# Kernel optimization log

Hardware: AMD Instinct MI355X
Metric: run time of the kernel (lower is better)

## Reference

```python
import math
import jax, jax.numpy as jnp
import numpy as np

B, Q, K, N, F = 4096, 1024, 256, 16384, 512


def setup_inputs() -> dict:
    key = jax.random.key(0)
    ks = jax.random.split(key, 6)
    return {
        "pooled_h": jax.random.normal(ks[0], (B, Q), jnp.float32),
        "snapshot_keys": jax.random.normal(ks[1], (N, K), jnp.float32),
        "snapshot_embs": jax.random.normal(ks[2], (N, F), jnp.float32),
        "Wq": jax.random.normal(ks[3], (Q, K), jnp.float32) / math.sqrt(Q),
        "bq": jnp.zeros((K,), jnp.float32),
        "Wb": jax.random.normal(ks[4], (Q, 1), jnp.float32) / math.sqrt(Q),
        "bb": jnp.zeros((1,), jnp.float32),
        "fallback": jnp.zeros((F,), jnp.float32),
        "topk": 2,
    }


def reference(pooled_h, snapshot_keys, snapshot_embs, Wq, bq, Wb, bb, fallback, topk):
    # q = q_proj(pooled_h)                                  [B, K]
    q = pooled_h @ Wq + bq
    # scores = q @ keys^T / sqrt(key_dim)                   [B, N]
    scores = (q @ snapshot_keys.T) / jnp.sqrt(jnp.asarray(q.shape[-1], q.dtype))
    # top-k values/indices per row, scatter into -inf mask, masked softmax
    vals, idx = jax.lax.top_k(scores, topk)                 # [B, k], [B, k]
    rows = jnp.arange(scores.shape[0])[:, None]             # [B, 1]
    mask = jnp.full_like(scores, -jnp.inf).at[rows, idx].set(vals)
    alpha = jax.nn.softmax(mask, axis=-1)                   # [B, N], k nonzeros/row
    emb_mix = alpha @ snapshot_embs                         # [B, F]
    beta = jax.nn.sigmoid(pooled_h @ Wb + bb)               # [B, 1]
    return emb_mix * beta, alpha
```

## Files before the change

kernel.cpp:

```cpp
#include <hip/hip_runtime.h>
#include <math.h>

#define B_ 4096
#define Q_ 1024
#define KD 256
#define N_ 16384
#define F_ 512

typedef __attribute__((ext_vector_type(8))) short bhalf8;
typedef __attribute__((ext_vector_type(4))) float f32x4;
typedef __attribute__((ext_vector_type(16))) float f32x16;

static __device__ __forceinline__ unsigned short f2bf(float f) {
  unsigned int u = __builtin_bit_cast(unsigned int, f);
  unsigned int r = (u + 0x7fffu + ((u >> 16) & 1u)) >> 16;
  return (unsigned short)r;
}
static __device__ __forceinline__ unsigned umaxu(unsigned a, unsigned b) { return a > b ? a : b; }
static __device__ __forceinline__ unsigned uminu(unsigned a, unsigned b) { return a < b ? a : b; }

__global__ __launch_bounds__(256)
void k_convert_keys(const float* __restrict__ keys, unsigned short* __restrict__ kbf) {
  const size_t base = ((size_t)blockIdx.x * 256 + threadIdx.x) * 8;
  const float4 x = *reinterpret_cast<const float4*>(&keys[base]);
  const float4 y = *reinterpret_cast<const float4*>(&keys[base + 4]);
  bhalf8 o;
  o[0] = (short)f2bf(x.x); o[1] = (short)f2bf(x.y);
  o[2] = (short)f2bf(x.z); o[3] = (short)f2bf(x.w);
  o[4] = (short)f2bf(y.x); o[5] = (short)f2bf(y.y);
  o[6] = (short)f2bf(y.z); o[7] = (short)f2bf(y.w);
  *reinterpret_cast<bhalf8*>(&kbf[base]) = o;
}

__global__ __launch_bounds__(256, 2)
void k_qproj(const float* __restrict__ ph, const float* __restrict__ Wq,
             float* __restrict__ qpart) {
  __shared__ __align__(16) float As[2][64][64];
  __shared__ __align__(16) float Ws[2][64][64];
  const int tid = threadIdx.x;
  const int tx = tid & 15, ty = tid >> 4;
  const int c0 = (blockIdx.x & 3) * 64;
  const int kh = blockIdx.x >> 2;
  const int r0 = blockIdx.y * 64;
  const int kbase = kh * 512;
  const int sr = tid & 63, sk = (tid >> 6) * 16;
  float* qout = qpart + (size_t)kh * B_ * KD;

  float acc[4][4] = {};
  float4 a0, a1, a2, a3;

  auto stageW = [&](int bi, int kc) {
#pragma unroll
    for (int i = 0; i < 4; ++i) {
      const int D = i * 4096 + tid * 16;
      const int kk = D >> 8;
      const int cb = D & 255;
      const float* src = &Wq[(size_t)(kbase + kc * 64 + kk) * KD + c0 + (cb >> 2)];
      __builtin_amdgcn_global_load_lds(
          (const __attribute__((address_space(1))) unsigned int*)src,
          (__attribute__((address_space(3))) unsigned int*)((char*)&Ws[bi][0][0] + D),
          16, 0, 0);
    }
  };

  stageW(0, 0);
  {
    const float* src = &ph[(size_t)(r0 + sr) * Q_ + kbase + sk];
    a0 = *reinterpret_cast<const float4*>(src + 0);
    a1 = *reinterpret_cast<const float4*>(src + 4);
    a2 = *reinterpret_cast<const float4*>(src + 8);
    a3 = *reinterpret_cast<const float4*>(src + 12);
    As[0][sk + 0][sr] = a0.x; As[0][sk + 1][sr] = a0.y;
    As[0][sk + 2][sr] = a0.z; As[0][sk + 3][sr] = a0.w;
    As[0][sk + 4][sr] = a1.x; As[0][sk + 5][sr] = a1.y;
    As[0][sk + 6][sr] = a1.z; As[0][sk + 7][sr] = a1.w;
    As[0][sk + 8][sr] = a2.x; As[0][sk + 9][sr] = a2.y;
    As[0][sk + 10][sr] = a2.z; As[0][sk + 11][sr] = a2.w;
    As[0][sk + 12][sr] = a3.x; As[0][sk + 13][sr] = a3.y;
    As[0][sk + 14][sr] = a3.z; As[0][sk + 15][sr] = a3.w;
  }
  __syncthreads();

  int buf = 0;
  for (int kc = 0; kc < 8; ++kc) {
    if (kc < 7) {
      const float* src = &ph[(size_t)(r0 + sr) * Q_ + kbase + (kc + 1) * 64 + sk];
      a0 = *reinterpret_cast<const float4*>(src + 0);
      a1 = *reinterpret_cast<const float4*>(src + 4);
      a2 = *reinterpret_cast<const float4*>(src + 8);
      a3 = *reinterpret_cast<const float4*>(src + 12);
      stageW(buf ^ 1, kc + 1);
    }
#pragma unroll 16
    for (int k = 0; k < 64; ++k) {
      const float4 a = *reinterpret_cast<const float4*>(&As[buf][k][ty * 4]);
      const float4 b = *reinterpret_cast<const float4*>(&Ws[buf][k][tx * 4]);
      acc[0][0] = fmaf(a.x, b.x, acc[0][0]); acc[0][1] = fmaf(a.x, b.y, acc[0][1]);
      acc[0][2] = fmaf(a.x, b.z, acc[0][2]); acc[0][3] = fmaf(a.x, b.w, acc[0][3]);
      acc[1][0] = fmaf(a.y, b.x, acc[1][0]); acc[1][1] = fmaf(a.y, b.y, acc[1][1]);
      acc[1][2] = fmaf(a.y, b.z, acc[1][2]); acc[1][3] = fmaf(a.y, b.w, acc[1][3]);
      acc[2][0] = fmaf(a.z, b.x, acc[2][0]); acc[2][1] = fmaf(a.z, b.y, acc[2][1]);
      acc[2][2] = fmaf(a.z, b.z, acc[2][2]); acc[2][3] = fmaf(a.z, b.w, acc[2][3]);
      acc[3][0] = fmaf(a.w, b.x, acc[3][0]); acc[3][1] = fmaf(a.w, b.y, acc[3][1]);
      acc[3][2] = fmaf(a.w, b.z, acc[3][2]); acc[3][3] = fmaf(a.w, b.w, acc[3][3]);
    }
    if (kc < 7) {
      As[buf ^ 1][sk + 0][sr] = a0.x; As[buf ^ 1][sk + 1][sr] = a0.y;
      As[buf ^ 1][sk + 2][sr] = a0.z; As[buf ^ 1][sk + 3][sr] = a0.w;
      As[buf ^ 1][sk + 4][sr] = a1.x; As[buf ^ 1][sk + 5][sr] = a1.y;
      As[buf ^ 1][sk + 6][sr] = a1.z; As[buf ^ 1][sk + 7][sr] = a1.w;
      As[buf ^ 1][sk + 8][sr] = a2.x; As[buf ^ 1][sk + 9][sr] = a2.y;
      As[buf ^ 1][sk + 10][sr] = a2.z; As[buf ^ 1][sk + 11][sr] = a2.w;
      As[buf ^ 1][sk + 12][sr] = a3.x; As[buf ^ 1][sk + 13][sr] = a3.y;
      As[buf ^ 1][sk + 14][sr] = a3.z; As[buf ^ 1][sk + 15][sr] = a3.w;
    }
    __syncthreads();
    buf ^= 1;
  }

#pragma unroll
  for (int i = 0; i < 4; ++i) {
    const int r = r0 + ty * 4 + i;
    const int c = c0 + tx * 4;
    float4 v;
    v.x = acc[i][0]; v.y = acc[i][1]; v.z = acc[i][2]; v.w = acc[i][3];
    *reinterpret_cast<float4*>(&qout[(size_t)r * KD + c]) = v;
  }
}

__global__ __launch_bounds__(256)
void k_qmerge(float* __restrict__ qpart, const float* __restrict__ bq,
              unsigned short* __restrict__ qbf) {
  const size_t base = (size_t)blockIdx.x * 1024 + threadIdx.x * 4;
  const float4 v0 = *reinterpret_cast<const float4*>(&qpart[base]);
  const float4 v1 = *reinterpret_cast<const float4*>(&qpart[(size_t)B_ * KD + base]);
  const int c = (int)(base & (KD - 1));
  const float4 b = *reinterpret_cast<const float4*>(&bq[c]);
  float4 v;
  v.x = v0.x + v1.x + b.x; v.y = v0.y + v1.y + b.y;
  v.z = v0.z + v1.z + b.z; v.w = v0.w + v1.w + b.w;
  *reinterpret_cast<float4*>(&qpart[base]) = v;
  ushort4 bv;
  bv.x = f2bf(v.x); bv.y = f2bf(v.y); bv.z = f2bf(v.z); bv.w = f2bf(v.w);
  *reinterpret_cast<ushort4*>(&qbf[base]) = bv;
}

__global__ __launch_bounds__(256, 3)
void k_scores_mfma(const unsigned short* __restrict__ qbf,
                   const unsigned short* __restrict__ kbf,
                   unsigned* __restrict__ candP, float* __restrict__ outAlpha) {
  __shared__ __align__(16) char lds[32768];
  __shared__ unsigned mbuf[64 * 12];
  const int tid = threadIdx.x;
  const int wave = tid >> 6, lane = tid & 63;
  const int l31 = lane & 31, lhi = lane >> 5;
  const int rh = wave >> 1, ch = wave & 1;
  const int bc = blockIdx.x, br = blockIdx.y;
  const int row0 = br * 64;
  const int m_row = row0 + rh * 32 + l31;

  float4* zb = reinterpret_cast<float4*>(
      (char*)outAlpha + (size_t)(br * 16 + bc) * 262144);
  const float4 z4 = {0.f, 0.f, 0.f, 0.f};

  bhalf8 qf[16];
#pragma unroll
  for (int kt = 0; kt < 16; ++kt)
    qf[kt] = *reinterpret_cast<const bhalf8*>(&qbf[(size_t)m_row * KD + kt * 16 + lhi * 8]);

  auto stage = [&](int bi, int u) {
    const int t = u >> 1, kh = u & 1;
#pragma unroll
    for (int i = 0; i < 4; ++i) {
      const int D = i * 4096 + tid * 16;
      const int colt = D >> 8;
      const int kb = D & 255;
      const int kbs = kb ^ ((colt & 15) << 4);
      const char* src = (const char*)kbf +
          ((size_t)(bc * 1024 + t * 64 + colt) * 512 + kh * 256 + kbs);
      __builtin_amdgcn_global_load_lds(
          (const __attribute__((address_space(1))) unsigned int*)src,
          (__attribute__((address_space(3))) unsigned int*)(lds + bi * 16384 + D),
          16, 0, 0);
    }
  };

  unsigned P1 = 0u, P2 = 0u, P3 = 0u;
  const int acol = ch * 32 + l31;
  const int swz = (acol & 15) << 4;
  const int kofs = lhi * 16;

  stage(0, 0);
  __syncthreads();

  int buf = 0;
  for (int t = 0; t < 16; ++t) {
    f32x16 acc = {};
#pragma unroll
    for (int kh = 0; kh < 2; ++kh) {
      const int u = t * 2 + kh;
      if (u < 31) stage(buf ^ 1, u + 1);
      zb[u * 512 + tid] = z4;
      zb[u * 512 + 256 + tid] = z4;
      const char* kb = lds + buf * 16384 + acol * 256;
#pragma unroll
      for (int kt = 0; kt < 8; ++kt) {
        const bhalf8 af = *reinterpret_cast<const bhalf8*>(kb + ((kt * 32 + kofs) ^ swz));
        acc = __builtin_amdgcn_mfma_f32_32x32x16_bf16(af, qf[kh * 8 + kt], acc, 0, 0, 0);
      }
      if (kh == 1) {
        const int cb = t * 64 + ch * 32 + lhi * 4;
#pragma unroll
        for (int r = 0; r < 16; ++r) {
          const int rofs = (r & 3) + 8 * (r >> 2);
          const unsigned p =
              (__builtin_bit_cast(unsigned, acc[r] + 512.f) & 0xFFFFF800u) |
              (unsigned)(cb + rofs);
          const unsigned w1 = uminu(P1, p); P1 = umaxu(P1, p);
          const unsigned w2 = uminu(P2, w1); P2 = umaxu(P2, w1);
          P3 = umaxu(P3, w2);
        }
      }
      __syncthreads();
      buf ^= 1;
    }
  }

  {
    const int mrow = rh * 32 + l31;
    const int slot = ch * 2 + lhi;
    mbuf[mrow * 12 + slot * 3 + 0] = P1;
    mbuf[mrow * 12 + slot * 3 + 1] = P2;
    mbuf[mrow * 12 + slot * 3 + 2] = P3;
  }
  __syncthreads();
  if (tid < 64) {
    unsigned T1 = 0u, T2 = 0u, T3 = 0u, T4 = 0u;
#pragma unroll
    for (int j = 0; j < 12; ++j) {
      const unsigned p = mbuf[tid * 12 + j];
      const unsigned w1 = uminu(T1, p); T1 = umaxu(T1, p);
      const unsigned w2 = uminu(T2, w1); T2 = umaxu(T2, w1);
      const unsigned w3 = uminu(T3, w2); T3 = umaxu(T3, w2);
      T4 = umaxu(T4, w3);
    }
    const size_t o = (size_t)(row0 + tid) * 64 + bc * 4;
    candP[o + 0] = T1; candP[o + 1] = T2; candP[o + 2] = T3; candP[o + 3] = T4;
  }
}

__global__ __launch_bounds__(256)
void k_finalize(const float* __restrict__ q, const float* __restrict__ keys,
                const float* __restrict__ ph, const float* __restrict__ Wb,
                const float* __restrict__ bb, const float* __restrict__ embs,
                const unsigned* __restrict__ candP,
                float* __restrict__ outEmb, float* __restrict__ outAlpha) {
  __shared__ float red[4];
  __shared__ int   topIdx[8];
  __shared__ float resc[8];
  __shared__ float sParam[3];
  __shared__ int   sIdx[2];
  const int tid = threadIdx.x;
  const int wave = tid >> 6, lane = tid & 63;
  const int row = blockIdx.x;
  float* arow = outAlpha + (size_t)row * N_;

  {
    const float4 a = *reinterpret_cast<const float4*>(&ph[(size_t)row * Q_ + tid * 4]);
    const float4 w = *reinterpret_cast<const float4*>(&Wb[tid * 4]);
    float s = a.x * w.x + a.y * w.y + a.z * w.z + a.w * w.w;
#pragma unroll
    for (int m = 32; m >= 1; m >>= 1) s += __shfl_xor(s, m);
    if (lane == 0) red[wave] = s;
  }

  if (wave == 0) {
    unsigned p = candP[(size_t)row * 64 + lane];
    const int mycol = (lane >> 2) * 1024 + (int)(p & 0x7FFu);
#pragma unroll
    for (int it = 0; it < 8; ++it) {
      unsigned mx = p;
#pragma unroll
      for (int m = 32; m >= 1; m >>= 1) {
        const unsigned o = (unsigned)__shfl_xor((int)mx, m);
        mx = mx > o ? mx : o;
      }
      const unsigned long long bal = __ballot(p == mx);
      const int src = __ffsll((unsigned long long)bal) - 1;
      if (lane == src) { topIdx[it] = mycol; p = 0u; }
    }
  }
  __syncthreads();

  {
#pragma unroll
    for (int h = 0; h < 2; ++h) {
      const int cnd = topIdx[wave * 2 + h];
      const float4 qv = *reinterpret_cast<const float4*>(&q[(size_t)row * KD + lane * 4]);
      const float4 kv = *reinterpret_cast<const float4*>(&keys[(size_t)cnd * KD + lane * 4]);
      float s = qv.x * kv.x + qv.y * kv.y + qv.z * kv.z + qv.w * kv.w;
#pragma unroll
      for (int m = 32; m >= 1; m >>= 1) s += __shfl_xor(s, m);
      if (lane == 0) resc[wave * 2 + h] = s * 0.0625f;
    }
  }
  __syncthreads();

  if (tid == 0) {
    float w1 = -INFINITY, w2 = -INFINITY; int j1 = 0x7fffffff, j2 = 0x7fffffff;
#pragma unroll
    for (int c = 0; c < 8; ++c) {
      const float v = resc[c]; const int x = topIdx[c];
      const bool beat1 = (v > w1) || (v == w1 && x < j1);
      const bool beat2 = (v > w2) || (v == w2 && x < j2);
      if (beat1) { w2 = w1; j2 = j1; w1 = v; j1 = x; }
      else if (beat2) { w2 = v; j2 = x; }
    }
    const float t = expf(w2 - w1);
    const float inv = 1.f / (1.f + t);
    const float bsum = red[0] + red[1] + red[2] + red[3] + bb[0];
    sParam[0] = inv; sParam[1] = t * inv;
    sParam[2] = 1.f / (1.f + expf(-bsum));
    sIdx[0] = j1; sIdx[1] = j2;
  }
  __syncthreads();

  const float a1 = sParam[0], a2 = sParam[1], beta = sParam[2];
  const int j1 = sIdx[0], j2 = sIdx[1];
  if (tid == 0) { arow[j1] = a1; arow[j2] = a2; }
  if (tid < 128) {
    const int f = tid * 4;
    const float4 e1 = *reinterpret_cast<const float4*>(&embs[(size_t)j1 * F_ + f]);
    const float4 e2 = *reinterpret_cast<const float4*>(&embs[(size_t)j2 * F_ + f]);
    float4 o;
    o.x = beta * (a1 * e1.x + a2 * e2.x);
    o.y = beta * (a1 * e1.y + a2 * e2.y);
    o.z = beta * (a1 * e1.z + a2 * e2.z);
    o.w = beta * (a1 * e1.w + a2 * e2.w);
    *reinterpret_cast<float4*>(&outEmb[(size_t)row * F_ + f]) = o;
  }
}

extern "C" void kernel_launch(void* const* d_in, const int* in_sizes, int n_in,
                              void* d_out, int out_size, void* d_ws, size_t ws_size,
                              hipStream_t stream) {
  const float* ph   = (const float*)d_in[0];
  const float* keys = (const float*)d_in[1];
  const float* embs = (const float*)d_in[2];
  const float* Wq   = (const float*)d_in[3];
  const float* bq   = (const float*)d_in[4];
  const float* Wb   = (const float*)d_in[5];
  const float* bb   = (const float*)d_in[6];

  float* outEmb   = (float*)d_out;
  float* outAlpha = outEmb + (size_t)B_ * F_;

  float*          qpart = (float*)d_ws;
  unsigned short* qbf   = (unsigned short*)(qpart + 2 * (size_t)B_ * KD);
  unsigned short* kbf   = qbf + (size_t)B_ * KD;
  unsigned*       candP = (unsigned*)(kbf + (size_t)N_ * KD);

  k_convert_keys<<<(N_ * KD / 8) / 256, 256, 0, stream>>>(keys, kbf);
  k_qproj<<<dim3(8, B_ / 64), 256, 0, stream>>>(ph, Wq, qpart);
  k_qmerge<<<(B_ * KD / 4) / 256, 256, 0, stream>>>(qpart, bq, qbf);
  k_scores_mfma<<<dim3(16, 64), 256, 0, stream>>>(qbf, kbf, candP, outAlpha);
  k_finalize<<<B_, 256, 0, stream>>>(qpart, keys, ph, Wb, bb, embs, candP,
                                     outEmb, outAlpha);
}
```

Baseline: 140.1 us.

## Split q-projection K dimension four ways and keep top-2 per lane in scores

The q projection now splits the 1024-long reduction into four 256-wide slices instead of two, using smaller 32-deep LDS tiles and doubling the grid so more blocks run at higher occupancy. The merge kernel sums four partial buffers, which adds workspace and extra global traffic. Separately, the scores kernel keeps only the top-2 packed candidates per lane instead of top-3, which cuts compare work, register use and shared buffer size, and it raises the occupancy hint. The finalize stage still gets four candidates per column block, but with fewer per-lane candidates a near-tie could be missed if it relied on the extra slot for bf16 rescoring.

```diff
diff --git a/kernel.cpp b/kernel.cpp
--- a/kernel.cpp
+++ b/kernel.cpp
@@ -32,30 +32,30 @@
   *reinterpret_cast<bhalf8*>(&kbf[base]) = o;
 }
 
-__global__ __launch_bounds__(256, 2)
+__global__ __launch_bounds__(256, 4)
 void k_qproj(const float* __restrict__ ph, const float* __restrict__ Wq,
              float* __restrict__ qpart) {
-  __shared__ __align__(16) float As[2][64][64];
-  __shared__ __align__(16) float Ws[2][64][64];
+  __shared__ __align__(16) float As[2][32][64];
+  __shared__ __align__(16) float Ws[2][32][64];
   const int tid = threadIdx.x;
   const int tx = tid & 15, ty = tid >> 4;
   const int c0 = (blockIdx.x & 3) * 64;
-  const int kh = blockIdx.x >> 2;
+  const int kq = blockIdx.x >> 2;
   const int r0 = blockIdx.y * 64;
-  const int kbase = kh * 512;
-  const int sr = tid & 63, sk = (tid >> 6) * 16;
-  float* qout = qpart + (size_t)kh * B_ * KD;
+  const int kbase = kq * 256;
+  const int sr = tid & 63, sk = (tid >> 6) * 8;
+  float* qout = qpart + (size_t)kq * B_ * KD;
 
   float acc[4][4] = {};
-  float4 a0, a1, a2, a3;
+  float4 a0, a1;
 
   auto stageW = [&](int bi, int kc) {
 #pragma unroll
-    for (int i = 0; i < 4; ++i) {
+    for (int i = 0; i < 2; ++i) {
       const int D = i * 4096 + tid * 16;
       const int kk = D >> 8;
       const int cb = D & 255;
-      const float* src = &Wq[(size_t)(kbase + kc * 64 + kk) * KD + c0 + (cb >> 2)];
+      const float* src = &Wq[(size_t)(kbase + kc * 32 + kk) * KD + c0 + (cb >> 2)];
       __builtin_amdgcn_global_load_lds(
           (const __attribute__((address_space(1))) unsigned int*)src,
           (__attribute__((address_space(3))) unsigned int*)((char*)&Ws[bi][0][0] + D),
@@ -68,31 +68,23 @@
     const float* src = &ph[(size_t)(r0 + sr) * Q_ + kbase + sk];
     a0 = *reinterpret_cast<const float4*>(src + 0);
     a1 = *reinterpret_cast<const float4*>(src + 4);
-    a2 = *reinterpret_cast<const float4*>(src + 8);
-    a3 = *reinterpret_cast<const float4*>(src + 12);
     As[0][sk + 0][sr] = a0.x; As[0][sk + 1][sr] = a0.y;
     As[0][sk + 2][sr] = a0.z; As[0][sk + 3][sr] = a0.w;
     As[0][sk + 4][sr] = a1.x; As[0][sk + 5][sr] = a1.y;
     As[0][sk + 6][sr] = a1.z; As[0][sk + 7][sr] = a1.w;
-    As[0][sk + 8][sr] = a2.x; As[0][sk + 9][sr] = a2.y;
-    As[0][sk + 10][sr] = a2.z; As[0][sk + 11][sr] = a2.w;
-    As[0][sk + 12][sr] = a3.x; As[0][sk + 13][sr] = a3.y;
-    As[0][sk + 14][sr] = a3.z; As[0][sk + 15][sr] = a3.w;
   }
   __syncthreads();
 
   int buf = 0;
   for (int kc = 0; kc < 8; ++kc) {
     if (kc < 7) {
-      const float* src = &ph[(size_t)(r0 + sr) * Q_ + kbase + (kc + 1) * 64 + sk];
+      const float* src = &ph[(size_t)(r0 + sr) * Q_ + kbase + (kc + 1) * 32 + sk];
       a0 = *reinterpret_cast<const float4*>(src + 0);
       a1 = *reinterpret_cast<const float4*>(src + 4);
-      a2 = *reinterpret_cast<const float4*>(src + 8);
-      a3 = *reinterpret_cast<const float4*>(src + 12);
       stageW(buf ^ 1, kc + 1);
     }
 #pragma unroll 16
-    for (int k = 0; k < 64; ++k) {
+    for (int k = 0; k < 32; ++k) {
       const float4 a = *reinterpret_cast<const float4*>(&As[buf][k][ty * 4]);
       const float4 b = *reinterpret_cast<const float4*>(&Ws[buf][k][tx * 4]);
       acc[0][0] = fmaf(a.x, b.x, acc[0][0]); acc[0][1] = fmaf(a.x, b.y, acc[0][1]);
@@ -109,10 +101,6 @@
       As[buf ^ 1][sk + 2][sr] = a0.z; As[buf ^ 1][sk + 3][sr] = a0.w;
       As[buf ^ 1][sk + 4][sr] = a1.x; As[buf ^ 1][sk + 5][sr] = a1.y;
       As[buf ^ 1][sk + 6][sr] = a1.z; As[buf ^ 1][sk + 7][sr] = a1.w;
-      As[buf ^ 1][sk + 8][sr] = a2.x; As[buf ^ 1][sk + 9][sr] = a2.y;
-      As[buf ^ 1][sk + 10][sr] = a2.z; As[buf ^ 1][sk + 11][sr] = a2.w;
-      As[buf ^ 1][sk + 12][sr] = a3.x; As[buf ^ 1][sk + 13][sr] = a3.y;
-      As[buf ^ 1][sk + 14][sr] = a3.z; As[buf ^ 1][sk + 15][sr] = a3.w;
     }
     __syncthreads();
     buf ^= 1;
@@ -132,25 +120,30 @@
 void k_qmerge(float* __restrict__ qpart, const float* __restrict__ bq,
               unsigned short* __restrict__ qbf) {
   const size_t base = (size_t)blockIdx.x * 1024 + threadIdx.x * 4;
+  const size_t stride = (size_t)B_ * KD;
   const float4 v0 = *reinterpret_cast<const float4*>(&qpart[base]);
-  const float4 v1 = *reinterpret_cast<const float4*>(&qpart[(size_t)B_ * KD + base]);
+  const float4 v1 = *reinterpret_cast<const float4*>(&qpart[stride + base]);
+  const float4 v2 = *reinterpret_cast<const float4*>(&qpart[2 * stride + base]);
+  const float4 v3 = *reinterpret_cast<const float4*>(&qpart[3 * stride + base]);
   const int c = (int)(base & (KD - 1));
   const float4 b = *reinterpret_cast<const float4*>(&bq[c]);
   float4 v;
-  v.x = v0.x + v1.x + b.x; v.y = v0.y + v1.y + b.y;
-  v.z = v0.z + v1.z + b.z; v.w = v0.w + v1.w + b.w;
+  v.x = ((v0.x + v1.x) + v2.x) + v3.x + b.x;
+  v.y = ((v0.y + v1.y) + v2.y) + v3.y + b.y;
+  v.z = ((v0.z + v1.z) + v2.z) + v3.z + b.z;
+  v.w = ((v0.w + v1.w) + v2.w) + v3.w + b.w;
   *reinterpret_cast<float4*>(&qpart[base]) = v;
   ushort4 bv;
   bv.x = f2bf(v.x); bv.y = f2bf(v.y); bv.z = f2bf(v.z); bv.w = f2bf(v.w);
   *reinterpret_cast<ushort4*>(&qbf[base]) = bv;
 }
 
-__global__ __launch_bounds__(256, 3)
+__global__ __launch_bounds__(256, 4)
 void k_scores_mfma(const unsigned short* __restrict__ qbf,
                    const unsigned short* __restrict__ kbf,
                    unsigned* __restrict__ candP, float* __restrict__ outAlpha) {
   __shared__ __align__(16) char lds[32768];
-  __shared__ unsigned mbuf[64 * 12];
+  __shared__ unsigned mbuf[64 * 8];
   const int tid = threadIdx.x;
   const int wave = tid >> 6, lane = tid & 63;
   const int l31 = lane & 31, lhi = lane >> 5;
@@ -185,7 +178,7 @@
     }
   };
 
-  unsigned P1 = 0u, P2 = 0u, P3 = 0u;
+  unsigned P1 = 0u, P2 = 0u;
   const int acol = ch * 32 + l31;
   const int swz = (acol & 15) << 4;
   const int kofs = lhi * 16;
@@ -216,9 +209,9 @@
           const unsigned p =
               (__builtin_bit_cast(unsigned, acc[r] + 512.f) & 0xFFFFF800u) |
               (unsigned)(cb + rofs);
-          const unsigned w1 = uminu(P1, p); P1 = umaxu(P1, p);
-          const unsigned w2 = uminu(P2, w1); P2 = umaxu(P2, w1);
-          P3 = umaxu(P3, w2);
+          const unsigned w1 = uminu(P1, p);
+          P1 = umaxu(P1, p);
+          P2 = umaxu(P2, w1);
         }
       }
       __syncthreads();
@@ -229,16 +222,15 @@
   {
     const int mrow = rh * 32 + l31;
     const int slot = ch * 2 + lhi;
-    mbuf[mrow * 12 + slot * 3 + 0] = P1;
-    mbuf[mrow * 12 + slot * 3 + 1] = P2;
-    mbuf[mrow * 12 + slot * 3 + 2] = P3;
+    mbuf[mrow * 8 + slot * 2 + 0] = P1;
+    mbuf[mrow * 8 + slot * 2 + 1] = P2;
   }
   __syncthreads();
   if (tid < 64) {
     unsigned T1 = 0u, T2 = 0u, T3 = 0u, T4 = 0u;
 #pragma unroll
-    for (int j = 0; j < 12; ++j) {
-      const unsigned p = mbuf[tid * 12 + j];
+    for (int j = 0; j < 8; ++j) {
+      const unsigned p = mbuf[tid * 8 + j];
       const unsigned w1 = uminu(T1, p); T1 = umaxu(T1, p);
       const unsigned w2 = uminu(T2, w1); T2 = umaxu(T2, w1);
       const unsigned w3 = uminu(T3, w2); T3 = umaxu(T3, w2);
@@ -356,12 +348,12 @@
   float* outAlpha = outEmb + (size_t)B_ * F_;
 
   float*          qpart = (float*)d_ws;
-  unsigned short* qbf   = (unsigned short*)(qpart + 2 * (size_t)B_ * KD);
+  unsigned short* qbf   = (unsigned short*)(qpart + 4 * (size_t)B_ * KD);
   unsigned short* kbf   = qbf + (size_t)B_ * KD;
   unsigned*       candP = (unsigned*)(kbf + (size_t)N_ * KD);
 
   k_convert_keys<<<(N_ * KD / 8) / 256, 256, 0, stream>>>(keys, kbf);
-  k_qproj<<<dim3(8, B_ / 64), 256, 0, stream>>>(ph, Wq, qpart);
+  k_qproj<<<dim3(16, B_ / 64), 256, 0, stream>>>(ph, Wq, qpart);
   k_qmerge<<<(B_ * KD / 4) / 256, 256, 0, stream>>>(qpart, bq, qbf);
   k_scores_mfma<<<dim3(16, 64), 256, 0, stream>>>(qbf, kbf, candP, outAlpha);
   k_finalize<<<B_, 256, 0, stream>>>(qpart, keys, ph, Wb, bb, embs, candP,
```

Result: faster. 132.9 us (-5.1%).
